# Optimization experiments

Measured on AMD Instinct MI355X. Metric: run time of the kernel, lower is better.

## Reference

```python
import jax, jax.numpy as jnp
import numpy as np

B, DIMS, SIZE = 8, 512, 64
C = DIMS // 2
EPS = 1e-5


def setup_inputs() -> dict:
    key = jax.random.key(0)
    ks = jax.random.split(key, 24)
    f = lambda k, s, sc=0.05: jax.random.normal(k, s, dtype=jnp.float32) * sc
    return {
        "x": jax.random.normal(ks[0], (B, DIMS, SIZE, SIZE), dtype=jnp.float32),
        "cv1_w": f(ks[1], (C, DIMS)),
        "bn1_g": 1.0 + f(ks[2], (C,)),
        "bn1_b": f(ks[3], (C,)),
        "bn1_m": f(ks[4], (C,)),
        "bn1_v": 1.0 + 0.1 * jax.random.uniform(ks[5], (C,), dtype=jnp.float32),
        "q_w": f(ks[6], (C, C)), "q_b": f(ks[7], (C,)),
        "k_w": f(ks[8], (C, C)), "k_b": f(ks[9], (C,)),
        "v_w": f(ks[10], (C, C)), "v_b": f(ks[11], (C,)),
        "e_w": f(ks[12], (C, C)), "e_b": f(ks[13], (C,)),
        "rel_h": f(ks[14], (1, C, SIZE, 1), 1.0) * 0.05,
        "rel_w": f(ks[15], (1, C, 1, SIZE), 1.0) * 0.05,
        "cv2_w": f(ks[16], (DIMS, C)),
        "bn2_g": 1.0 + f(ks[17], (DIMS,)),
        "bn2_b": f(ks[18], (DIMS,)),
        "bn2_m": f(ks[19], (DIMS,)),
        "bn2_v": 1.0 + 0.1 * jax.random.uniform(ks[20], (DIMS,), dtype=jnp.float32),
    }


def _conv1x1(h, w):
    # 1x1 conv == channel contraction
    return jnp.einsum('oc,bchw->bohw', w, h)


def _bn(h, g, b, m, v):
    scale = g / jnp.sqrt(v + EPS)
    return (h - m[None, :, None, None]) * scale[None, :, None, None] + b[None, :, None, None]


def reference(x, cv1_w, bn1_g, bn1_b, bn1_m, bn1_v,
              q_w, q_b, k_w, k_b, v_w, v_b, e_w, e_b,
              rel_h, rel_w, cv2_w, bn2_g, bn2_b, bn2_m, bn2_v):
    x1 = jax.nn.silu(_bn(_conv1x1(x, cv1_w), bn1_g, bn1_b, bn1_m, bn1_v))  # [B,C,H,W]
    Bq, Cc, H, W = x1.shape
    N = H * W

    def proj(w, b):
        return (_conv1x1(x1, w) + b[None, :, None, None]).reshape(Bq, Cc, N)

    q = proj(q_w, q_b)
    k = proj(k_w, k_b)
    v = proj(v_w, v_b)
    e = proj(e_w, e_b)

    # content-content: q^T k  -> [B, N, N]
    cc = jnp.einsum('bcn,bcm->bnm', q, k)
    # content-position: (rel_h + rel_w) broadcast to [C,H,W] -> [C,N]; pos^T @ e
    pos = (rel_h + rel_w).reshape(Cc, N)
    cp = jnp.einsum('cn,bcm->bnm', pos, e)

    attn = jax.nn.softmax(cc + cp, axis=-1)  # [B,N,N]
    # out = v @ attn^T  -> [B,C,N]
    out = jnp.einsum('bcm,bnm->bcn', v, attn).reshape(Bq, Cc, H, W)

    y = jax.nn.silu(_bn(_conv1x1(out, cv2_w), bn2_g, bn2_b, bn2_m, bn2_v))
    return x + y
```

## Files before the change

### kernel.cpp

```cpp
#include <hip/hip_runtime.h>


typedef __bf16 bf16;
typedef __attribute__((ext_vector_type(8))) __bf16 bf16x8;
typedef __attribute__((ext_vector_type(4))) __bf16 bf16x4;
typedef __attribute__((ext_vector_type(4))) float f32x4;

__device__ __forceinline__ float silu_f(float x) { return x / (1.f + __expf(-x)); }

__device__ __forceinline__ void zero_acc(f32x4 (&acc)[4][4])
{
#pragma unroll
    for (int i = 0; i < 4; ++i)
#pragma unroll
        for (int j = 0; j < 4; ++j)
            acc[i][j] = (f32x4){0.f, 0.f, 0.f, 0.f};
}

__device__ __forceinline__ void load_lds16(const bf16* g, bf16* l)
{
    __builtin_amdgcn_global_load_lds(
        (const __attribute__((address_space(1))) unsigned int*)g,
        (__attribute__((address_space(3))) unsigned int*)l, 16, 0, 0);
}

__device__ __forceinline__ void wg_barrier()
{
    asm volatile("" ::: "memory");
    __builtin_amdgcn_s_barrier();
    asm volatile("" ::: "memory");
}

__device__ __forceinline__ void gemm_core_db(
    const bf16* __restrict__ A, int lda,
    const bf16* __restrict__ B, int ldb,
    int K, f32x4 (&acc)[4][4])
{
    __shared__ bf16 As[2][128 * 32];
    __shared__ bf16 Bs[2][128 * 32];
    const int tid = threadIdx.x;
    const int wave = tid >> 6;
    const int lane = tid & 63;
    const int lm = lane & 15;
    const int kq = lane >> 4;
    const int m0 = (wave >> 1) * 64;
    const int n0 = (wave & 1) * 64;
    const int srow = tid >> 2;
    const int skoff = (((tid & 3) ^ ((tid >> 3) & 3))) * 8;
    const int krd = (kq ^ ((lm >> 1) & 3)) * 8;
    zero_acc(acc);
    const bf16* ga = A + (size_t)srow * lda + skoff;
    const bf16* gb = B + (size_t)srow * ldb + skoff;
    load_lds16(ga, As[0] + tid * 8);
    load_lds16(ga + (size_t)64 * lda, As[0] + tid * 8 + 64 * 32);
    load_lds16(gb, Bs[0] + tid * 8);
    load_lds16(gb + (size_t)64 * ldb, Bs[0] + tid * 8 + 64 * 32);
    const int nt = K >> 5;
    for (int t = 0; t < nt; ++t) {
        const int cur = t & 1;
        if (t + 1 < nt) {
            const bf16* na = ga + (t + 1) * 32;
            const bf16* nb = gb + (t + 1) * 32;
            bf16* dA = As[cur ^ 1] + tid * 8;
            bf16* dB = Bs[cur ^ 1] + tid * 8;
            load_lds16(na, dA);
            load_lds16(na + (size_t)64 * lda, dA + 64 * 32);
            load_lds16(nb, dB);
            load_lds16(nb + (size_t)64 * ldb, dB + 64 * 32);
            asm volatile("s_waitcnt vmcnt(4)" ::: "memory");
        } else {
            asm volatile("s_waitcnt vmcnt(0)" ::: "memory");
        }
        wg_barrier();
        const bf16* as = As[cur];
        const bf16* bs = Bs[cur];
        bf16x8 av[4], bv[4];
#pragma unroll
        for (int tt = 0; tt < 4; ++tt)
            av[tt] = *(const bf16x8*)(as + (m0 + tt * 16 + lm) * 32 + krd);
#pragma unroll
        for (int tt = 0; tt < 4; ++tt)
            bv[tt] = *(const bf16x8*)(bs + (n0 + tt * 16 + lm) * 32 + krd);
#pragma unroll
        for (int i = 0; i < 4; ++i)
#pragma unroll
            for (int j = 0; j < 4; ++j)
                acc[i][j] = __builtin_amdgcn_mfma_f32_16x16x32_bf16(
                    av[i], bv[j], acc[i][j], 0, 0, 0);
        wg_barrier();
    }
}

__device__ __forceinline__ void gemm_core_256(
    const bf16* __restrict__ A, int lda,
    const bf16* __restrict__ B, int ldb,
    int K, f32x4 (&acc)[8][4])
{
    __shared__ bf16 As[2][16384];
    __shared__ bf16 Bs[2][16384];
    const int tid = threadIdx.x;
    const int lane = tid & 63;
    const int wid = tid >> 6;
    const int wm = wid >> 2, wn = wid & 3;
    const int lm = lane & 15, kq = lane >> 4;
    const int srow = tid >> 3;
    const int skoff = ((tid & 7) ^ (srow & 7)) * 8;
    const bf16* ga = A + (size_t)srow * lda + skoff;
    const bf16* gb = B + (size_t)srow * ldb + skoff;
#pragma unroll
    for (int r = 0; r < 4; ++r)
        load_lds16(ga + (size_t)(64 * r) * lda, As[0] + tid * 8 + r * 4096);
#pragma unroll
    for (int r = 0; r < 4; ++r)
        load_lds16(gb + (size_t)(64 * r) * ldb, Bs[0] + tid * 8 + r * 4096);
#pragma unroll
    for (int i = 0; i < 8; ++i)
#pragma unroll
        for (int j = 0; j < 4; ++j)
            acc[i][j] = (f32x4){0.f, 0.f, 0.f, 0.f};
    const int nt = K >> 6;
    for (int t = 0; t < nt; ++t) {
        const int cur = t & 1;
        if (t + 1 < nt) {
            const bf16* na = ga + (t + 1) * 64;
            const bf16* nb = gb + (t + 1) * 64;
#pragma unroll
            for (int r = 0; r < 4; ++r)
                load_lds16(na + (size_t)(64 * r) * lda,
                           As[cur ^ 1] + tid * 8 + r * 4096);
#pragma unroll
            for (int r = 0; r < 4; ++r)
                load_lds16(nb + (size_t)(64 * r) * ldb,
                           Bs[cur ^ 1] + tid * 8 + r * 4096);
            asm volatile("s_waitcnt vmcnt(8)" ::: "memory");
        } else {
            asm volatile("s_waitcnt vmcnt(0)" ::: "memory");
        }
        wg_barrier();
        const bf16* as = As[cur];
        const bf16* bs = Bs[cur];
#pragma unroll
        for (int ks = 0; ks < 2; ++ks) {
            bf16x8 av[8], bv[4];
#pragma unroll
            for (int i = 0; i < 8; ++i) {
                int lr = wm * 128 + i * 16 + lm;
                av[i] = *(const bf16x8*)(as + lr * 64 +
                                         (((ks << 2) | kq) ^ (lr & 7)) * 8);
            }
#pragma unroll
            for (int j = 0; j < 4; ++j) {
                int lr = wn * 64 + j * 16 + lm;
                bv[j] = *(const bf16x8*)(bs + lr * 64 +
                                         (((ks << 2) | kq) ^ (lr & 7)) * 8);
            }
            __builtin_amdgcn_s_setprio(1);
#pragma unroll
            for (int i = 0; i < 8; ++i)
#pragma unroll
                for (int j = 0; j < 4; ++j)
                    acc[i][j] = __builtin_amdgcn_mfma_f32_16x16x32_bf16(
                        av[i], bv[j], acc[i][j], 0, 0, 0);
            __builtin_amdgcn_s_setprio(0);
        }
        wg_barrier();
    }
}


__global__ __launch_bounds__(256) void prep_misc_kernel(
    const float* __restrict__ cv1_w,
    const float* __restrict__ qw, const float* __restrict__ qb,
    const float* __restrict__ kw, const float* __restrict__ kb,
    const float* __restrict__ vw, const float* __restrict__ vb,
    const float* __restrict__ ew, const float* __restrict__ eb,
    const float* __restrict__ cv2_w,
    const float* __restrict__ g1, const float* __restrict__ b1,
    const float* __restrict__ m1, const float* __restrict__ v1,
    const float* __restrict__ g2, const float* __restrict__ b2,
    const float* __restrict__ m2, const float* __restrict__ v2,
    const float* __restrict__ rel_h, const float* __restrict__ rel_w,
    bf16* __restrict__ w1b, bf16* __restrict__ wqkve, bf16* __restrict__ w2b,
    bf16* __restrict__ posT,
    float* __restrict__ biasq,
    float* __restrict__ bn1s, float* __restrict__ bn1h,
    float* __restrict__ bn2s, float* __restrict__ bn2h)
{
    int idx = blockIdx.x * 256 + threadIdx.x;
    if (idx < 131072) { w1b[idx] = (bf16)cv1_w[idx]; return; }
    idx -= 131072;
    if (idx < 262144) {
        int j = idx >> 8, c = idx & 255;
        int p = j >> 8, r = j & 255;
        const float* w = (p == 0) ? qw : (p == 1) ? kw : (p == 2) ? vw : ew;
        wqkve[idx] = (bf16)w[r * 256 + c];
        return;
    }
    idx -= 262144;
    if (idx < 131072) { w2b[idx] = (bf16)cv2_w[idx]; return; }
    idx -= 131072;
    if (idx < 1024) {
        int p = idx >> 8, r = idx & 255;
        const float* bb = (p == 0) ? qb : (p == 1) ? kb : (p == 2) ? vb : eb;
        biasq[idx] = bb[r];
        return;
    }
    idx -= 1024;
    if (idx < 256) {
        float s = g1[idx] * rsqrtf(v1[idx] + 1e-5f);
        bn1s[idx] = s;
        bn1h[idx] = b1[idx] - m1[idx] * s;
        return;
    }
    idx -= 256;
    if (idx < 512) {
        float s = g2[idx] * rsqrtf(v2[idx] + 1e-5f);
        bn2s[idx] = s;
        bn2h[idx] = b2[idx] - m2[idx] * s;
        return;
    }
    idx -= 512;
    if (idx < 32768) {
        int r = idx >> 8, c = idx & 255;
        posT[idx] = (bf16)((r < 64) ? rel_h[c * 64 + r] : rel_w[c * 64 + (r - 64)]);
        return;
    }
}

__global__ __launch_bounds__(256) void transpose_x_kernel(
    const float* __restrict__ x, bf16* __restrict__ xt)
{
    __shared__ float tile[64][65];
    int b = blockIdx.z;
    int n0 = blockIdx.x * 64;
    int d0 = blockIdx.y * 64;
    int tx = threadIdx.x & 63, ty = threadIdx.x >> 6;
#pragma unroll
    for (int i = 0; i < 16; ++i) {
        int d = i * 4 + ty;
        tile[d][tx] = x[((size_t)(b * 512 + d0 + d)) * 4096 + n0 + tx];
    }
    __syncthreads();
#pragma unroll
    for (int i = 0; i < 16; ++i) {
        int n = i * 4 + ty;
        xt[((size_t)(b * 4096 + n0 + n)) * 512 + d0 + tx] = (bf16)tile[tx][n];
    }
}

__global__ __launch_bounds__(256) void transpose_v_kernel(
    const bf16* __restrict__ v_nm, bf16* __restrict__ v_cm)
{
    __shared__ float tile[64][65];
    int b = blockIdx.z;
    int m0 = blockIdx.x * 64;
    int c0 = blockIdx.y * 64;
    int tx = threadIdx.x & 63, ty = threadIdx.x >> 6;
#pragma unroll
    for (int i = 0; i < 16; ++i) {
        int m = i * 4 + ty;
        tile[m][tx] = (float)v_nm[((size_t)(b * 4096 + m0 + m)) * 256 + c0 + tx];
    }
    __syncthreads();
#pragma unroll
    for (int i = 0; i < 16; ++i) {
        int c = i * 4 + ty;
        v_cm[((size_t)(b * 256 + c0 + c)) * 4096 + m0 + tx] = (bf16)tile[tx][c];
    }
}


__global__ __launch_bounds__(256) void gemm1_kernel(
    const bf16* __restrict__ xt, const bf16* __restrict__ w1b,
    const float* __restrict__ bn1s, const float* __restrict__ bn1h,
    bf16* __restrict__ x1t)
{
    const bf16* A = xt + (size_t)(blockIdx.y * 128) * 512;
    const bf16* Bm = w1b + (size_t)(blockIdx.x * 128) * 512;
    f32x4 acc[4][4];
    gemm_core_db(A, 512, Bm, 512, 512, acc);
    int wave = threadIdx.x >> 6;
    int lane = threadIdx.x & 63;
    int m0 = blockIdx.y * 128 + (wave >> 1) * 64;
    int n0 = blockIdx.x * 128 + (wave & 1) * 64;
    int lm = lane & 15, kq = lane >> 4;
#pragma unroll
    for (int i = 0; i < 4; ++i)
#pragma unroll
        for (int j = 0; j < 4; ++j)
#pragma unroll
            for (int r = 0; r < 4; ++r) {
                int row = m0 + i * 16 + kq * 4 + r;
                int col = n0 + j * 16 + lm;
                float h = bn1s[col] * acc[i][j][r] + bn1h[col];
                x1t[(size_t)row * 256 + col] = (bf16)silu_f(h);
            }
}

__global__ __launch_bounds__(512, 1) void gemm2_kernel(
    const bf16* __restrict__ x1t, const bf16* __restrict__ wqkve,
    const float* __restrict__ biasq,
    bf16* __restrict__ qk, bf16* __restrict__ v_nm, bf16* __restrict__ e_nm)
{
    const int bx = blockIdx.x, by = blockIdx.y;
    const bf16* A = x1t + (size_t)(by * 256) * 256;
    const bf16* Bm = wqkve + (size_t)(bx * 256) * 256;
    f32x4 acc[8][4];
    gemm_core_256(A, 256, Bm, 256, 256, acc);
    const int tid = threadIdx.x, lane = tid & 63, wid = tid >> 6;
    const int wm = wid >> 2, wn = wid & 3, lm = lane & 15, kq = lane >> 4;
#pragma unroll
    for (int i = 0; i < 8; ++i)
#pragma unroll
        for (int j = 0; j < 4; ++j)
#pragma unroll
            for (int r = 0; r < 4; ++r) {
                int row = by * 256 + wm * 128 + i * 16 + kq * 4 + r;
                int col = bx * 256 + wn * 64 + j * 16 + lm;
                bf16 val = (bf16)(acc[i][j][r] + biasq[col]);
                if (bx < 2)          qk[(size_t)row * 512 + col] = val;
                else if (bx == 2)    v_nm[(size_t)row * 256 + (col - 512)] = val;
                else                 e_nm[(size_t)row * 256 + (col - 768)] = val;
            }
}

__global__ __launch_bounds__(256) void gemm_rhw_kernel(
    const bf16* __restrict__ posT, const bf16* __restrict__ e_nm,
    bf16* __restrict__ rhw)
{
    int b = blockIdx.z;
    const bf16* Bm = e_nm + ((size_t)b * 4096 + blockIdx.x * 128) * 256;
    f32x4 acc[4][4];
    gemm_core_db(posT, 256, Bm, 256, 256, acc);
    int wave = threadIdx.x >> 6;
    int lane = threadIdx.x & 63;
    int m0 = (wave >> 1) * 64, n0 = (wave & 1) * 64;
    int lm = lane & 15, kq = lane >> 4;
    bf16* rb = rhw + (size_t)b * 128 * 4096 + blockIdx.x * 128;
#pragma unroll
    for (int i = 0; i < 4; ++i)
#pragma unroll
        for (int j = 0; j < 4; ++j)
#pragma unroll
            for (int r = 0; r < 4; ++r)
                rb[(size_t)(m0 + i * 16 + kq * 4 + r) * 4096 + n0 + j * 16 + lm] =
                    (bf16)acc[i][j][r];
}

__global__ __launch_bounds__(512, 1) void attn_kernel(
    const bf16* __restrict__ qk, const bf16* __restrict__ v_cm,
    const bf16* __restrict__ rhw, bf16* __restrict__ out_t)
{
    __shared__ bf16 Qs[32768];
    __shared__ bf16 KV[2][8192];
    __shared__ bf16 Ps[16384];
    __shared__ float rs[128];
    const int flat = blockIdx.x;
    const int b = flat & 7, by = flat >> 3;
    const int tid = threadIdx.x;
    const int lane = tid & 63, wid = tid >> 6;
    const int lm = lane & 15, kq = lane >> 4;
    const int wmS = wid >> 2, wqS = wid & 3;
    const int wqP = wid >> 2, wcP = wid & 3;
    if (tid < 128) rs[tid] = 0.f;

    const bf16* qbase = qk + ((size_t)(b * 4096 + by * 128)) * 512;
    const bf16* kbase = qk + (size_t)b * 4096 * 512 + 256;
    const bf16* vbase = v_cm + (size_t)b * 256 * 4096;
    const bf16* rhb   = rhw + (size_t)b * 128 * 4096;

#pragma unroll
    for (int r = 0; r < 8; ++r) {
        int q = (tid >> 5) + r * 16;
        int cs = tid & 31;
        load_lds16(qbase + (size_t)q * 512 + ((cs ^ (q & 7)) << 3),
                   Qs + tid * 8 + r * 4096);
    }

    f32x4 acc_o[4][4];
#pragma unroll
    for (int i = 0; i < 4; ++i)
#pragma unroll
        for (int j = 0; j < 4; ++j)
            acc_o[i][j] = (f32x4){0.f, 0.f, 0.f, 0.f};
    float rsum_p[2] = {0.f, 0.f};

    auto stageK = [&](int mb, int ct, int buf) {
#pragma unroll
        for (int r = 0; r < 2; ++r) {
            int row = (tid >> 3) + r * 64;
            int cs = tid & 7;
            load_lds16(kbase + (size_t)(mb + row) * 512 + ct * 64
                           + ((cs ^ (row & 7)) << 3),
                       KV[buf] + tid * 8 + r * 4096);
        }
    };
    auto stageV = [&](int mb, int ms, int buf) {
#pragma unroll
        for (int r = 0; r < 2; ++r) {
            int row = (tid >> 2) + r * 128;
            int cs = tid & 3;
            load_lds16(vbase + (size_t)row * 4096 + mb + ms * 32
                           + ((cs ^ ((row >> 1) & 3)) << 3),
                       KV[buf] + tid * 8 + r * 4096);
        }
    };

#pragma unroll 1
    for (int mt = 0; mt < 32; ++mt) {
        const int mb = mt * 128;
        f32x4 acc_s[4][2];
#pragma unroll
        for (int i = 0; i < 4; ++i)
#pragma unroll
            for (int j = 0; j < 2; ++j)
                acc_s[i][j] = (f32x4){0.f, 0.f, 0.f, 0.f};

        auto compS = [&](int ct, int buf) {
            const bf16* ks = KV[buf];
#pragma unroll
            for (int k2 = 0; k2 < 2; ++k2) {
                bf16x8 av[4], bv[2];
#pragma unroll
                for (int i = 0; i < 4; ++i) {
                    int mr = wmS * 64 + i * 16 + lm;
                    av[i] = *(const bf16x8*)(ks + mr * 64 +
                                             (((k2 << 2) | kq) ^ (mr & 7)) * 8);
                }
#pragma unroll
                for (int j = 0; j < 2; ++j) {
                    int qr = wqS * 32 + j * 16 + lm;
                    bv[j] = *(const bf16x8*)(Qs + qr * 256 +
                        (((ct << 3) | (k2 << 2) | kq) ^ (qr & 7)) * 8);
                }
                __builtin_amdgcn_s_setprio(1);
#pragma unroll
                for (int i = 0; i < 4; ++i)
#pragma unroll
                    for (int j = 0; j < 2; ++j)
                        acc_s[i][j] = __builtin_amdgcn_mfma_f32_16x16x32_bf16(
                            av[i], bv[j], acc_s[i][j], 0, 0, 0);
                __builtin_amdgcn_s_setprio(0);
            }
        };
        auto compPV = [&](int ms, int buf) {
            const bf16* vs = KV[buf];
            bf16x8 pa[4], vv[4];
#pragma unroll
            for (int i = 0; i < 4; ++i) {
                int qr = wqP * 64 + i * 16 + lm;
                pa[i] = *(const bf16x8*)(Ps + qr * 128 +
                                         (((ms << 2) | kq) ^ (qr & 7)) * 8);
            }
#pragma unroll
            for (int j = 0; j < 4; ++j) {
                int cr = wcP * 64 + j * 16 + lm;
                vv[j] = *(const bf16x8*)(vs + cr * 32 +
                                         (kq ^ ((cr >> 1) & 3)) * 8);
            }
            __builtin_amdgcn_s_setprio(1);
#pragma unroll
            for (int i = 0; i < 4; ++i)
#pragma unroll
                for (int j = 0; j < 4; ++j)
                    acc_o[i][j] = __builtin_amdgcn_mfma_f32_16x16x32_bf16(
                        pa[i], vv[j], acc_o[i][j], 0, 0, 0);
            __builtin_amdgcn_s_setprio(0);
        };

        stageK(mb, 0, 0); stageK(mb, 1, 1);
        asm volatile("s_waitcnt vmcnt(2)" ::: "memory"); wg_barrier();
        compS(0, 0); wg_barrier();
        stageK(mb, 2, 0);
        asm volatile("s_waitcnt vmcnt(2)" ::: "memory"); wg_barrier();
        compS(1, 1); wg_barrier();
        stageK(mb, 3, 1);
        asm volatile("s_waitcnt vmcnt(2)" ::: "memory"); wg_barrier();
        bf16x4 rh4[2][4], rw4[2][4];
#pragma unroll
        for (int j = 0; j < 2; ++j) {
            int hj = by * 2 + ((wqS * 32 + j * 16) >= 64 ? 1 : 0);
            int wj = (wqS * 32 + j * 16 + lm) & 63;
#pragma unroll
            for (int i = 0; i < 4; ++i) {
                int mo = mb + wmS * 64 + i * 16 + kq * 4;
                rh4[j][i] = *(const bf16x4*)(rhb + (size_t)hj * 4096 + mo);
                rw4[j][i] = *(const bf16x4*)(rhb + (size_t)(64 + wj) * 4096 + mo);
            }
        }
        compS(2, 0); wg_barrier();
        asm volatile("s_waitcnt vmcnt(0)" ::: "memory"); wg_barrier();
        compS(3, 1);
#pragma unroll
        for (int i = 0; i < 4; ++i)
#pragma unroll
            for (int j = 0; j < 2; ++j) {
                bf16x4 pk;
#pragma unroll
                for (int r = 0; r < 4; ++r) {
                    float sv = acc_s[i][j][r] + (float)rh4[j][i][r]
                                              + (float)rw4[j][i][r];
                    float e = __expf(sv - 8.f);
                    rsum_p[j] += e;
                    pk[r] = (bf16)e;
                }
                int q = wqS * 32 + j * 16 + lm;
                int ck = wmS * 8 + i * 2 + (kq >> 1);
                *(bf16x4*)((char*)Ps + q * 256 + ((ck ^ (q & 7)) << 4)
                           + ((kq & 1) << 3)) = pk;
            }
        asm volatile("s_waitcnt lgkmcnt(0)" ::: "memory");
        wg_barrier();
        stageV(mb, 0, 0); stageV(mb, 1, 1);
        asm volatile("s_waitcnt vmcnt(2)" ::: "memory"); wg_barrier();
        compPV(0, 0); wg_barrier();
        stageV(mb, 2, 0);
        asm volatile("s_waitcnt vmcnt(2)" ::: "memory"); wg_barrier();
        compPV(1, 1); wg_barrier();
        stageV(mb, 3, 1);
        asm volatile("s_waitcnt vmcnt(2)" ::: "memory"); wg_barrier();
        compPV(2, 0); wg_barrier();
        asm volatile("s_waitcnt vmcnt(0)" ::: "memory"); wg_barrier();
        compPV(3, 1); wg_barrier();
    }

#pragma unroll
    for (int j = 0; j < 2; ++j) {
        rsum_p[j] += __shfl_xor(rsum_p[j], 16);
        rsum_p[j] += __shfl_xor(rsum_p[j], 32);
    }
    if (kq == 0) {
#pragma unroll
        for (int j = 0; j < 2; ++j)
            atomicAdd(&rs[wqS * 32 + j * 16 + lm], rsum_p[j]);
    }
    __syncthreads();
    bf16* ob = out_t + ((size_t)(b * 4096 + by * 128)) * 256;
#pragma unroll
    for (int i = 0; i < 4; ++i)
#pragma unroll
        for (int r = 0; r < 4; ++r) {
            int q = wqP * 64 + i * 16 + kq * 4 + r;
            float inv = 1.f / rs[q];
#pragma unroll
            for (int j = 0; j < 4; ++j)
                ob[(size_t)q * 256 + wcP * 64 + j * 16 + lm] =
                    (bf16)(acc_o[i][j][r] * inv);
        }
}

__global__ __launch_bounds__(512, 1) void gemm5_kernel(
    const bf16* __restrict__ w2b, const bf16* __restrict__ out_t,
    const float* __restrict__ bn2s, const float* __restrict__ bn2h,
    const float* __restrict__ x, float* __restrict__ out)
{
    int b = blockIdx.z;
    const bf16* A = w2b + (size_t)(blockIdx.y * 256) * 256;
    const bf16* Bm = out_t + ((size_t)b * 4096 + blockIdx.x * 256) * 256;
    f32x4 acc[8][4];
    gemm_core_256(A, 256, Bm, 256, 256, acc);
    const int tid = threadIdx.x, lane = tid & 63, wid = tid >> 6;
    const int wm = wid >> 2, wn = wid & 3, lm = lane & 15, kq = lane >> 4;
#pragma unroll
    for (int i = 0; i < 8; ++i)
#pragma unroll
        for (int j = 0; j < 4; ++j)
#pragma unroll
            for (int r = 0; r < 4; ++r) {
                int d = blockIdx.y * 256 + wm * 128 + i * 16 + kq * 4 + r;
                int n = blockIdx.x * 256 + wn * 64 + j * 16 + lm;
                float h = bn2s[d] * acc[i][j][r] + bn2h[d];
                size_t gi = ((size_t)(b * 512 + d)) * 4096 + n;
                out[gi] = x[gi] + silu_f(h);
            }
}


extern "C" void kernel_launch(void* const* d_in, const int* in_sizes, int n_in,
                              void* d_out, int out_size, void* d_ws, size_t ws_size,
                              hipStream_t stream)
{
    (void)in_sizes; (void)n_in; (void)out_size; (void)ws_size;
    const float* x     = (const float*)d_in[0];
    const float* cv1_w = (const float*)d_in[1];
    const float* bn1_g = (const float*)d_in[2];
    const float* bn1_b = (const float*)d_in[3];
    const float* bn1_m = (const float*)d_in[4];
    const float* bn1_v = (const float*)d_in[5];
    const float* q_w   = (const float*)d_in[6];
    const float* q_b   = (const float*)d_in[7];
    const float* k_w   = (const float*)d_in[8];
    const float* k_b   = (const float*)d_in[9];
    const float* v_w   = (const float*)d_in[10];
    const float* v_b   = (const float*)d_in[11];
    const float* e_w   = (const float*)d_in[12];
    const float* e_b   = (const float*)d_in[13];
    const float* rel_h = (const float*)d_in[14];
    const float* rel_w = (const float*)d_in[15];
    const float* cv2_w = (const float*)d_in[16];
    const float* bn2_g = (const float*)d_in[17];
    const float* bn2_b = (const float*)d_in[18];
    const float* bn2_m = (const float*)d_in[19];
    const float* bn2_v = (const float*)d_in[20];
    float* out = (float*)d_out;

    char* ws = (char*)d_ws;
    bf16* xt    = (bf16*)(ws + 0);
    bf16* x1t   = (bf16*)(ws + 33554432);
    bf16* v_nm  = (bf16*)(ws + 50331648);
    bf16* e_nm  = (bf16*)(ws + 67108864);
    bf16* qk    = (bf16*)(ws + 134217728);
    bf16* v_cm  = (bf16*)(ws + 167772160);
    bf16* rhw   = (bf16*)(ws + 184549376);
    bf16* out_t = (bf16*)(ws + 192937984);
    bf16* w1b   = (bf16*)(ws + 209715200);
    bf16* wqkve = (bf16*)(ws + 209977344);
    bf16* w2b   = (bf16*)(ws + 210501632);
    bf16* posT  = (bf16*)(ws + 210763776);
    float* biasq= (float*)(ws + 210829312);
    float* bn1s = (float*)(ws + 210833408);
    float* bn1h = (float*)(ws + 210834432);
    float* bn2s = (float*)(ws + 210835456);
    float* bn2h = (float*)(ws + 210837504);

    prep_misc_kernel<<<2183, 256, 0, stream>>>(
        cv1_w, q_w, q_b, k_w, k_b, v_w, v_b, e_w, e_b, cv2_w,
        bn1_g, bn1_b, bn1_m, bn1_v, bn2_g, bn2_b, bn2_m, bn2_v,
        rel_h, rel_w,
        w1b, wqkve, w2b, posT, biasq, bn1s, bn1h, bn2s, bn2h);
    transpose_x_kernel<<<dim3(64, 8, 8), 256, 0, stream>>>(x, xt);
    gemm1_kernel<<<dim3(2, 256), 256, 0, stream>>>(xt, w1b, bn1s, bn1h, x1t);
    gemm2_kernel<<<dim3(4, 128), 512, 0, stream>>>(x1t, wqkve, biasq, qk, v_nm, e_nm);
    gemm_rhw_kernel<<<dim3(32, 1, 8), 256, 0, stream>>>(posT, e_nm, rhw);
    transpose_v_kernel<<<dim3(64, 4, 8), 256, 0, stream>>>(v_nm, v_cm);
    attn_kernel<<<256, 512, 0, stream>>>(qk, v_cm, rhw, out_t);
    gemm5_kernel<<<dim3(16, 2, 8), 512, 0, stream>>>(w2b, out_t, bn2s, bn2h, x, out);
}
```

Before: 506.9 us.

## Hold Q in registers and pipeline K/V loads through a four-slot LDS ring

The attention kernel now keeps each wave's Q fragments in registers instead of staging the whole Q tile in shared memory. K and V chunks stream through a four-slot LDS ring, so V loads overlap the later score MFMAs and the next tile's K loads overlap the PV MFMAs. Several barriers and wait points are removed. Launch bounds now request two blocks per CU, which tightens the register budget while Q, the S accumulators and the O accumulators are all live, so register spills are possible.

```diff
diff --git a/kernel.cpp b/kernel.cpp
--- a/kernel.cpp
+++ b/kernel.cpp
@@ -347,12 +347,11 @@
                     (bf16)acc[i][j][r];
 }
 
-__global__ __launch_bounds__(512, 1) void attn_kernel(
+__global__ __launch_bounds__(512, 2) void attn_kernel(
     const bf16* __restrict__ qk, const bf16* __restrict__ v_cm,
     const bf16* __restrict__ rhw, bf16* __restrict__ out_t)
 {
-    __shared__ bf16 Qs[32768];
-    __shared__ bf16 KV[2][8192];
+    __shared__ bf16 RING[4][8192];
     __shared__ bf16 Ps[16384];
     __shared__ float rs[128];
     const int flat = blockIdx.x;
@@ -369,13 +368,16 @@
     const bf16* vbase = v_cm + (size_t)b * 256 * 4096;
     const bf16* rhb   = rhw + (size_t)b * 128 * 4096;
 
-#pragma unroll
-    for (int r = 0; r < 8; ++r) {
-        int q = (tid >> 5) + r * 16;
-        int cs = tid & 31;
-        load_lds16(qbase + (size_t)q * 512 + ((cs ^ (q & 7)) << 3),
-                   Qs + tid * 8 + r * 4096);
-    }
+    bf16x8 qreg[4][2][2];
+#pragma unroll
+    for (int ct = 0; ct < 4; ++ct)
+#pragma unroll
+        for (int k2 = 0; k2 < 2; ++k2)
+#pragma unroll
+            for (int j = 0; j < 2; ++j)
+                qreg[ct][k2][j] = *(const bf16x8*)(
+                    qbase + (size_t)(wqS * 32 + j * 16 + lm) * 512
+                          + ct * 64 + k2 * 32 + kq * 8);
 
     f32x4 acc_o[4][4];
 #pragma unroll
@@ -385,26 +387,29 @@
             acc_o[i][j] = (f32x4){0.f, 0.f, 0.f, 0.f};
     float rsum_p[2] = {0.f, 0.f};
 
-    auto stageK = [&](int mb, int ct, int buf) {
+    auto stageK = [&](int mb, int ct, bf16* dst) {
 #pragma unroll
         for (int r = 0; r < 2; ++r) {
             int row = (tid >> 3) + r * 64;
             int cs = tid & 7;
             load_lds16(kbase + (size_t)(mb + row) * 512 + ct * 64
                            + ((cs ^ (row & 7)) << 3),
-                       KV[buf] + tid * 8 + r * 4096);
+                       dst + tid * 8 + r * 4096);
         }
     };
-    auto stageV = [&](int mb, int ms, int buf) {
+    auto stageV = [&](int mb, int ms, bf16* dst) {
 #pragma unroll
         for (int r = 0; r < 2; ++r) {
             int row = (tid >> 2) + r * 128;
             int cs = tid & 3;
             load_lds16(vbase + (size_t)row * 4096 + mb + ms * 32
                            + ((cs ^ ((row >> 1) & 3)) << 3),
-                       KV[buf] + tid * 8 + r * 4096);
+                       dst + tid * 8 + r * 4096);
         }
     };
+
+    stageK(0, 0, RING[0]);
+    stageK(0, 1, RING[1]);
 
 #pragma unroll 1
     for (int mt = 0; mt < 32; ++mt) {
@@ -416,35 +421,27 @@
             for (int j = 0; j < 2; ++j)
                 acc_s[i][j] = (f32x4){0.f, 0.f, 0.f, 0.f};
 
-        auto compS = [&](int ct, int buf) {
-            const bf16* ks = KV[buf];
+        auto compS = [&](int ct, const bf16* ks) {
 #pragma unroll
             for (int k2 = 0; k2 < 2; ++k2) {
-                bf16x8 av[4], bv[2];
+                bf16x8 av[4];
 #pragma unroll
                 for (int i = 0; i < 4; ++i) {
                     int mr = wmS * 64 + i * 16 + lm;
                     av[i] = *(const bf16x8*)(ks + mr * 64 +
                                              (((k2 << 2) | kq) ^ (mr & 7)) * 8);
                 }
-#pragma unroll
-                for (int j = 0; j < 2; ++j) {
-                    int qr = wqS * 32 + j * 16 + lm;
-                    bv[j] = *(const bf16x8*)(Qs + qr * 256 +
-                        (((ct << 3) | (k2 << 2) | kq) ^ (qr & 7)) * 8);
-                }
                 __builtin_amdgcn_s_setprio(1);
 #pragma unroll
                 for (int i = 0; i < 4; ++i)
 #pragma unroll
                     for (int j = 0; j < 2; ++j)
                         acc_s[i][j] = __builtin_amdgcn_mfma_f32_16x16x32_bf16(
-                            av[i], bv[j], acc_s[i][j], 0, 0, 0);
+                            av[i], qreg[ct][k2][j], acc_s[i][j], 0, 0, 0);
                 __builtin_amdgcn_s_setprio(0);
             }
         };
-        auto compPV = [&](int ms, int buf) {
-            const bf16* vs = KV[buf];
+        auto compPV = [&](int ms, const bf16* vs) {
             bf16x8 pa[4], vv[4];
 #pragma unroll
             for (int i = 0; i < 4; ++i) {
@@ -468,14 +465,22 @@
             __builtin_amdgcn_s_setprio(0);
         };
 
-        stageK(mb, 0, 0); stageK(mb, 1, 1);
-        asm volatile("s_waitcnt vmcnt(2)" ::: "memory"); wg_barrier();
-        compS(0, 0); wg_barrier();
-        stageK(mb, 2, 0);
-        asm volatile("s_waitcnt vmcnt(2)" ::: "memory"); wg_barrier();
-        compS(1, 1); wg_barrier();
-        stageK(mb, 3, 1);
-        asm volatile("s_waitcnt vmcnt(2)" ::: "memory"); wg_barrier();
+        stageK(mb, 2, RING[2]);
+        asm volatile("s_waitcnt vmcnt(4)" ::: "memory");
+        wg_barrier();
+        compS(0, RING[0]);
+        stageK(mb, 3, RING[3]);
+        asm volatile("s_waitcnt vmcnt(4)" ::: "memory");
+        wg_barrier();
+        compS(1, RING[1]);
+        stageV(mb, 0, RING[0]);
+        asm volatile("s_waitcnt vmcnt(4)" ::: "memory");
+        wg_barrier();
+        compS(2, RING[2]);
+        stageV(mb, 1, RING[1]);
+        asm volatile("s_waitcnt vmcnt(4)" ::: "memory");
+        wg_barrier();
+        compS(3, RING[3]);
         bf16x4 rh4[2][4], rw4[2][4];
 #pragma unroll
         for (int j = 0; j < 2; ++j) {
@@ -488,9 +493,7 @@
                 rw4[j][i] = *(const bf16x4*)(rhb + (size_t)(64 + wj) * 4096 + mo);
             }
         }
-        compS(2, 0); wg_barrier();
-        asm volatile("s_waitcnt vmcnt(0)" ::: "memory"); wg_barrier();
-        compS(3, 1);
+        asm volatile("s_waitcnt vmcnt(0)" ::: "memory");
 #pragma unroll
         for (int i = 0; i < 4; ++i)
 #pragma unroll
@@ -510,18 +513,28 @@
                            + ((kq & 1) << 3)) = pk;
             }
         asm volatile("s_waitcnt lgkmcnt(0)" ::: "memory");
-        wg_barrier();
-        stageV(mb, 0, 0); stageV(mb, 1, 1);
-        asm volatile("s_waitcnt vmcnt(2)" ::: "memory"); wg_barrier();
-        compPV(0, 0); wg_barrier();
-        stageV(mb, 2, 0);
-        asm volatile("s_waitcnt vmcnt(2)" ::: "memory"); wg_barrier();
-        compPV(1, 1); wg_barrier();
-        stageV(mb, 3, 1);
-        asm volatile("s_waitcnt vmcnt(2)" ::: "memory"); wg_barrier();
-        compPV(2, 0); wg_barrier();
-        asm volatile("s_waitcnt vmcnt(0)" ::: "memory"); wg_barrier();
-        compPV(3, 1); wg_barrier();
+        stageV(mb, 2, RING[2]);
+        wg_barrier();
+        compPV(0, RING[0]);
+        stageV(mb, 3, RING[3]);
+        wg_barrier();
+        compPV(1, RING[1]);
+        if (mt + 1 < 32) {
+            stageK(mb + 128, 0, RING[0]);
+            asm volatile("s_waitcnt vmcnt(4)" ::: "memory");
+        } else {
+            asm volatile("s_waitcnt vmcnt(2)" ::: "memory");
+        }
+        wg_barrier();
+        compPV(2, RING[2]);
+        if (mt + 1 < 32) {
+            stageK(mb + 128, 1, RING[1]);
+            asm volatile("s_waitcnt vmcnt(4)" ::: "memory");
+        } else {
+            asm volatile("s_waitcnt vmcnt(0)" ::: "memory");
+        }
+        wg_barrier();
+        compPV(3, RING[3]);
     }
 
 #pragma unroll
```

New measurement: 470.0 us. -7.3%, faster.
